# Optimization experiments

Measured on AMD Instinct MI355X. Metric: run time of the kernel, lower is better.

## Reference

```python
import jax, jax.numpy as jnp
import numpy as np
from jax import lax

B, T = 16384, 10
CAR, REG, POI, WEEK, TIME = 500000, 10000, 64, 7, 1440
H, LBL = 256, 512


def setup_inputs() -> dict:
    key = jax.random.key(0)
    ks = jax.random.split(key, 32)
    p = lambda i, shp: jax.random.normal(ks[i], shp, jnp.float32) * 0.05
    d = {}
    d["region_idx"] = jax.random.randint(ks[0], (B, T), 0, REG)
    d["poi_idx"] = jax.random.randint(ks[1], (B, T), 0, POI)
    d["car_idx"] = jax.random.randint(ks[2], (B,), 0, CAR)
    d["week_idx"] = jax.random.randint(ks[3], (B,), 0, WEEK)
    d["time_idx"] = jax.random.randint(ks[4], (B,), 0, TIME)
    d["coords"] = jax.random.normal(ks[5], (B, T, 2), jnp.float32)
    d["region_tbl"] = p(6, (REG, 8))
    d["poi_tbl"] = p(7, (POI, 4))
    d["car_tbl"] = p(8, (CAR, 16))
    d["week_tbl"] = p(9, (WEEK, 3))
    d["time_tbl"] = p(10, (TIME, 8))
    d["W_rp"] = p(11, (12, 32)); d["b_rp"] = p(12, (32,))
    d["W_co"] = p(13, (2, 8));  d["b_co"] = p(14, (8,))
    d["conv_w"] = p(15, (3, 40, 32)); d["conv_b"] = p(16, (32,))
    # 2-layer LSTM (torch gate order i,f,g,o), input 59, hidden 256
    d["Wih0"] = p(17, (4 * H, 59)); d["Whh0"] = p(18, (4 * H, H))
    d["bih0"] = p(19, (4 * H,));    d["bhh0"] = p(20, (4 * H,))
    d["Wih1"] = p(21, (4 * H, H)); d["Whh1"] = p(22, (4 * H, H))
    d["bih1"] = p(23, (4 * H,));   d["bhh1"] = p(24, (4 * H,))
    d["W1"] = p(25, (H, 512));    d["b1"] = p(26, (512,))
    d["W2"] = p(27, (512, 1024)); d["b2"] = p(28, (1024,))
    d["W3"] = p(29, (1024, LBL)); d["b3"] = p(30, (LBL,))
    return d


def _lstm_layer(x, Wih, Whh, bih, bhh):
    Bx, Hh = x.shape[0], Whh.shape[1]
    bias = bih + bhh

    def step(carry, xt):
        h, c = carry
        g = xt @ Wih.T + h @ Whh.T + bias
        i, f, gg, o = jnp.split(g, 4, axis=-1)
        c = jax.nn.sigmoid(f) * c + jax.nn.sigmoid(i) * jnp.tanh(gg)
        h = jax.nn.sigmoid(o) * jnp.tanh(c)
        return (h, c), h

    h0 = jnp.zeros((Bx, Hh), x.dtype)
    _, hs = lax.scan(step, (h0, h0), jnp.swapaxes(x, 0, 1))
    return jnp.swapaxes(hs, 0, 1)


def reference(region_idx, poi_idx, car_idx, week_idx, time_idx, coords,
              region_tbl, poi_tbl, car_tbl, week_tbl, time_tbl,
              W_rp, b_rp, W_co, b_co, conv_w, conv_b,
              Wih0, Whh0, bih0, bhh0, Wih1, Whh1, bih1, bhh1,
              W1, b1, W2, b2, W3, b3):
    # batched embedding gathers (replaces per-item python-loop lookups)
    rp = jnp.concatenate([region_tbl[region_idx], poi_tbl[poi_idx]], -1)   # [B,T,12]
    nv = jnp.concatenate([rp @ W_rp + b_rp, coords @ W_co + b_co], -1)     # [B,T,40]
    conv = jax.nn.elu(
        lax.conv_general_dilated(nv, conv_w, (1,), 'VALID',
                                 dimension_numbers=('NWC', 'WIO', 'NWC')) + conv_b)  # [B,T-2,32]
    emb = jnp.tanh(jnp.concatenate(
        [car_tbl[car_idx], week_tbl[week_idx], time_tbl[time_idx]], -1))   # [B,27]
    x = jnp.concatenate(
        [conv, jnp.broadcast_to(emb[:, None, :], conv.shape[:2] + (27,))], -1)  # [B,T-2,59]
    h = _lstm_layer(x, Wih0, Whh0, bih0, bhh0)
    h = _lstm_layer(h, Wih1, Whh1, bih1, bhh1)
    last = h[:, -1, :]                                                     # [B,256]
    # nn.Sequential of three Linears with NO activations between
    return ((last @ W1 + b1) @ W2 + b2) @ W3 + b3                          # [B,LBL]
```

## Files before the change

### kernel.cpp

```cpp
#include <hip/hip_runtime.h>
#include <hip/hip_bf16.h>
#include <math.h>

#define B_SZ 16384
#define T_CONV 8
#define HID 256
#define SK 16

typedef __bf16 bf16x8 __attribute__((ext_vector_type(8)));
typedef float f32x4 __attribute__((ext_vector_type(4)));

__device__ __forceinline__ float fsigm(float x) { return 1.f / (1.f + __expf(-x)); }
__device__ __forceinline__ float ftanh(float x) {
    float t = __expf(-2.f * fabsf(x));
    float r = (1.f - t) / (1.f + t);
    return x >= 0.f ? r : -r;
}

#define FB_SAMPLES 4
#define CWS 132
__global__ __launch_bounds__(256) void feature_kernel(
    const int* __restrict__ region_idx, const int* __restrict__ poi_idx,
    const int* __restrict__ car_idx, const int* __restrict__ week_idx,
    const int* __restrict__ time_idx, const float* __restrict__ coords,
    const float* __restrict__ region_tbl, const float* __restrict__ poi_tbl,
    const float* __restrict__ car_tbl, const float* __restrict__ week_tbl,
    const float* __restrict__ time_tbl, const float* __restrict__ W_rp,
    const float* __restrict__ b_rp, const float* __restrict__ W_co,
    const float* __restrict__ b_co, const float* __restrict__ conv_w,
    const float* __restrict__ conv_b, __bf16* __restrict__ Xp)
{
    __shared__ __align__(16) float s_cwT[32][CWS];
    __shared__ __align__(16) float s_nv[FB_SAMPLES][10][40];
    __shared__ float s_emb[FB_SAMPLES][27];
    __shared__ float s_rp[FB_SAMPLES][10][12];

    int tid = threadIdx.x;
    for (int i = tid; i < 3840; i += 256) {
        int o = i & 31, rc = i >> 5;
        s_cwT[o][rc] = conv_w[i];
    }

    int s  = tid >> 6;
    int lt = tid & 63;
    int b  = blockIdx.x * FB_SAMPLES + s;

    if (lt < 27) {
        float v;
        if (lt < 16)      v = car_tbl[(size_t)car_idx[b] * 16 + lt];
        else if (lt < 19) v = week_tbl[week_idx[b] * 3 + (lt - 16)];
        else              v = time_tbl[time_idx[b] * 8 + (lt - 19)];
        s_emb[s][lt] = tanhf(v);
    }
    for (int i = lt; i < 120; i += 64) {
        int t = i / 12, k = i % 12;
        float v;
        if (k < 8) v = region_tbl[(size_t)region_idx[b * 10 + t] * 8 + k];
        else       v = poi_tbl[poi_idx[b * 10 + t] * 4 + (k - 8)];
        s_rp[s][t][k] = v;
    }
    __syncthreads();

    for (int i = lt; i < 400; i += 64) {
        int t = i / 40, j = i % 40;
        float acc;
        if (j < 32) {
            acc = b_rp[j];
            #pragma unroll
            for (int k = 0; k < 12; k++) acc += s_rp[s][t][k] * W_rp[k * 32 + j];
        } else {
            int j2 = j - 32;
            acc = b_co[j2] + coords[(size_t)(b * 10 + t) * 2 + 0] * W_co[j2]
                           + coords[(size_t)(b * 10 + t) * 2 + 1] * W_co[8 + j2];
        }
        s_nv[s][t][j] = acc;
    }
    __syncthreads();

    for (int i = lt; i < 256; i += 64) {
        int t = i >> 5, o = i & 31;
        float4 f4 = make_float4(0.f, 0.f, 0.f, 0.f);
        #pragma unroll
        for (int dt = 0; dt < 3; dt++)
            #pragma unroll
            for (int c4 = 0; c4 < 10; c4++) {
                float4 va = *(const float4*)&s_nv[s][t + dt][c4 * 4];
                float4 vw = *(const float4*)&s_cwT[o][dt * 40 + c4 * 4];
                f4.x += va.x * vw.x; f4.y += va.y * vw.y;
                f4.z += va.z * vw.z; f4.w += va.w * vw.w;
            }
        float acc = conv_b[o] + (f4.x + f4.y) + (f4.z + f4.w);
        acc = acc > 0.f ? acc : expm1f(acc);
        Xp[(size_t)(b * 8 + t) * 64 + o] = (__bf16)acc;
    }
    for (int i = lt; i < 216; i += 64) {
        int t = i / 27, j = i % 27;
        Xp[(size_t)(b * 8 + t) * 64 + 32 + j] = (__bf16)s_emb[s][j];
    }
    for (int i = lt; i < 40; i += 64) {
        int t = i / 5, j = i % 5;
        Xp[(size_t)(b * 8 + t) * 64 + 59 + j] = (__bf16)0.f;
    }
}

#define AST 40
__global__ __launch_bounds__(256, 2) void lstm_fused(
    const __bf16* __restrict__ A1, int lda1, int K1,
    const __bf16* __restrict__ A2, int lda2,
    const __bf16* __restrict__ WS,
    const float* __restrict__ bias, float* __restrict__ cst,
    __bf16* __restrict__ hb,
    int KT, int is_t0)
{
    __shared__ __align__(16) unsigned char smem[2 * 128 * AST * 2];
    __bf16* As = (__bf16*)smem;
    float*  GL = (float*)smem;

    int tid = threadIdx.x;
    int bm  = blockIdx.y * 128;
    int bnf = blockIdx.x * 4;
    int bn  = blockIdx.x * 64;
    int l   = tid & 63;
    int g   = tid >> 6;
    int fr  = l & 15;
    int fo  = (l >> 4) * 8;

    f32x4 acc[8][4] = {};

    int s_row  = tid >> 1;
    int s_half = tid & 1;

    auto asrc = [&](int kt) -> const __bf16* {
        int k0 = kt * 32;
        if (k0 < K1) return A1 + (size_t)(bm + s_row) * lda1 + k0 + s_half * 16;
        return A2 + (size_t)(bm + s_row) * lda2 + (k0 - K1) + s_half * 16;
    };
    const __bf16* wbase = WS + ((size_t)g * 16 + bnf) * 512 + (size_t)l * 8;

    {
        const __bf16* s = asrc(0);
        bf16x8 v0 = *(const bf16x8*)s;
        bf16x8 v1 = *(const bf16x8*)(s + 8);
        *(bf16x8*)&As[s_row * AST + s_half * 16]     = v0;
        *(bf16x8*)&As[s_row * AST + s_half * 16 + 8] = v1;
    }
    bf16x8 bcur[4];
    #pragma unroll
    for (int j = 0; j < 4; j++) bcur[j] = *(const bf16x8*)(wbase + j * 512);

    for (int kt = 0; kt < KT; kt++) {
        int cb = kt & 1;
        bf16x8 bnxt[4], an0, an1;
        if (kt + 1 < KT) {
            const __bf16* s = asrc(kt + 1);
            an0 = *(const bf16x8*)s;
            an1 = *(const bf16x8*)(s + 8);
            const __bf16* wb = wbase + (size_t)(kt + 1) * 32768;
            #pragma unroll
            for (int j = 0; j < 4; j++) bnxt[j] = *(const bf16x8*)(wb + j * 512);
        }
        __syncthreads();
        bf16x8 af[8];
        #pragma unroll
        for (int mf = 0; mf < 8; mf++)
            af[mf] = *(bf16x8*)&As[cb * 128 * AST + (mf * 16 + fr) * AST + fo];
        #pragma unroll
        for (int mf = 0; mf < 8; mf++)
            #pragma unroll
            for (int j = 0; j < 4; j++)
                acc[mf][j] = __builtin_amdgcn_mfma_f32_16x16x32_bf16(
                    af[mf], bcur[j], acc[mf][j], 0, 0, 0);
        if (kt + 1 < KT) {
            *(bf16x8*)&As[(cb ^ 1) * 128 * AST + s_row * AST + s_half * 16]     = an0;
            *(bf16x8*)&As[(cb ^ 1) * 128 * AST + s_row * AST + s_half * 16 + 8] = an1;
            #pragma unroll
            for (int j = 0; j < 4; j++) bcur[j] = bnxt[j];
        }
    }

    int rbase = (l >> 4) * 4;
    int prow  = tid >> 4;
    int pcol  = (tid & 15) * 4;
    f32x4 bs[4];
    #pragma unroll
    for (int gg = 0; gg < 4; gg++)
        bs[gg] = *(const f32x4*)&bias[gg * 256 + bn + pcol];

    #pragma unroll
    for (int mf = 0; mf < 8; mf++) {
        __syncthreads();
        #pragma unroll
        for (int j = 0; j < 4; j++)
            #pragma unroll
            for (int e = 0; e < 4; e++)
                GL[(g * 16 + rbase + e) * 68 + j * 16 + fr] = acc[mf][j][e];
        __syncthreads();

        size_t moff = ((size_t)bm + mf * 16 + prow) * 256 + bn + pcol;
        f32x4 gi = *(f32x4*)&GL[(0 * 16 + prow) * 68 + pcol];
        f32x4 gf = *(f32x4*)&GL[(1 * 16 + prow) * 68 + pcol];
        f32x4 gg = *(f32x4*)&GL[(2 * 16 + prow) * 68 + pcol];
        f32x4 go = *(f32x4*)&GL[(3 * 16 + prow) * 68 + pcol];
        f32x4 cold = {0.f, 0.f, 0.f, 0.f};
        if (!is_t0) cold = *(f32x4*)&cst[moff];
        f32x4 cn;
        union { unsigned short u[4]; unsigned long long v; } hx;
        #pragma unroll
        for (int q = 0; q < 4; q++) {
            float i_ = fsigm(gi[q] + bs[0][q]);
            float f_ = fsigm(gf[q] + bs[1][q]);
            float g_ = ftanh(gg[q] + bs[2][q]);
            float o_ = fsigm(go[q] + bs[3][q]);
            float c_ = f_ * cold[q] + i_ * g_;
            cn[q] = c_;
            float h_ = o_ * ftanh(c_);
            __bf16 hv = (__bf16)h_;
            hx.u[q] = *(unsigned short*)&hv;
        }
        *(f32x4*)&cst[moff] = cn;
        *(unsigned long long*)&hb[moff] = hx.v;
    }
}

__global__ __launch_bounds__(256, 2) void head_mfma(
    const __bf16* __restrict__ A,
    const __bf16* __restrict__ WS,
    const float* __restrict__ bias, float* __restrict__ out)
{
    __shared__ __align__(16) __bf16 As[2][128 * AST];

    int tid = threadIdx.x;
    int bm  = blockIdx.y * 128;
    int l   = tid & 63;
    int wv  = tid >> 6;
    int fr  = l & 15;
    int fo  = (l >> 4) * 8;
    int nfb = blockIdx.x * 16 + wv * 4;

    f32x4 acc[8][4] = {};

    int s_row  = tid >> 1;
    int s_half = tid & 1;
    const __bf16* abase = A + (size_t)(bm + s_row) * 256 + s_half * 16;
    const __bf16* wbase = WS + (size_t)nfb * 512 + (size_t)l * 8;

    {
        bf16x8 v0 = *(const bf16x8*)abase;
        bf16x8 v1 = *(const bf16x8*)(abase + 8);
        *(bf16x8*)&As[0][s_row * AST + s_half * 16]     = v0;
        *(bf16x8*)&As[0][s_row * AST + s_half * 16 + 8] = v1;
    }
    bf16x8 bcur[4];
    #pragma unroll
    for (int j = 0; j < 4; j++) bcur[j] = *(const bf16x8*)(wbase + j * 512);

    #pragma unroll
    for (int kt = 0; kt < 8; kt++) {
        int cb = kt & 1;
        bf16x8 bnxt[4], an0, an1;
        if (kt + 1 < 8) {
            const __bf16* s = abase + (kt + 1) * 32;
            an0 = *(const bf16x8*)s;
            an1 = *(const bf16x8*)(s + 8);
            const __bf16* wb = wbase + (size_t)(kt + 1) * 16384;
            #pragma unroll
            for (int j = 0; j < 4; j++) bnxt[j] = *(const bf16x8*)(wb + j * 512);
        }
        __syncthreads();
        bf16x8 af[8];
        #pragma unroll
        for (int mf = 0; mf < 8; mf++)
            af[mf] = *(bf16x8*)&As[cb][(mf * 16 + fr) * AST + fo];
        #pragma unroll
        for (int mf = 0; mf < 8; mf++)
            #pragma unroll
            for (int j = 0; j < 4; j++)
                acc[mf][j] = __builtin_amdgcn_mfma_f32_16x16x32_bf16(
                    af[mf], bcur[j], acc[mf][j], 0, 0, 0);
        if (kt + 1 < 8) {
            *(bf16x8*)&As[cb ^ 1][s_row * AST + s_half * 16]     = an0;
            *(bf16x8*)&As[cb ^ 1][s_row * AST + s_half * 16 + 8] = an1;
            #pragma unroll
            for (int j = 0; j < 4; j++) bcur[j] = bnxt[j];
        }
    }

    int rbase = (l >> 4) * 4;
    #pragma unroll
    for (int mf = 0; mf < 8; mf++) {
        #pragma unroll
        for (int j = 0; j < 4; j++) {
            int n = (nfb + j) * 16 + fr;
            float bv = bias[n];
            #pragma unroll
            for (int e = 0; e < 4; e++) {
                size_t m = (size_t)bm + mf * 16 + rbase + e;
                out[m * 512 + n] = acc[mf][j][e] + bv;
            }
        }
    }
}

__global__ __launch_bounds__(256) void gemm_nn_sk(
    const float* __restrict__ A, int lda, const float* __restrict__ Bm, int ldb,
    float* __restrict__ P, int M, int N, int K)
{
    __shared__ float As[16][68];
    __shared__ float Bs[16][68];
    int tid = threadIdx.x;
    int tx = tid & 15, ty = tid >> 4;
    int bm = blockIdx.y * 64, bn = blockIdx.x * 64;
    int klen = K / SK;
    int kbeg = blockIdx.z * klen;

    float acc[4][4] = {};

    for (int k0 = kbeg; k0 < kbeg + klen; k0 += 16) {
        for (int i = tid; i < 1024; i += 256) {
            int k = i & 15, m = i >> 4;
            As[k][m] = A[(size_t)(bm + m) * lda + k0 + k];
        }
        for (int i = tid; i < 1024; i += 256) {
            int n = i & 63, k = i >> 6;
            Bs[k][n] = Bm[(size_t)(k0 + k) * ldb + bn + n];
        }
        __syncthreads();
        #pragma unroll
        for (int kk = 0; kk < 16; kk++) {
            float4 a = *(const float4*)&As[kk][ty * 4];
            float4 b = *(const float4*)&Bs[kk][tx * 4];
            float av[4] = {a.x, a.y, a.z, a.w};
            float bv[4] = {b.x, b.y, b.z, b.w};
            #pragma unroll
            for (int i = 0; i < 4; i++)
                #pragma unroll
                for (int j = 0; j < 4; j++)
                    acc[i][j] += av[i] * bv[j];
        }
        __syncthreads();
    }

    float* Pd = P + (size_t)blockIdx.z * M * N;
    #pragma unroll
    for (int i = 0; i < 4; i++) {
        int m = bm + ty * 4 + i;
        #pragma unroll
        for (int j = 0; j < 4; j++) {
            int n = bn + tx * 4 + j;
            Pd[(size_t)m * N + n] = acc[i][j];
        }
    }
}

__global__ __launch_bounds__(256) void reduce_sk(
    const float* __restrict__ P, int MN, float* __restrict__ C)
{
    int i = blockIdx.x * 256 + threadIdx.x;
    if (i >= MN) return;
    float a = 0.f;
    #pragma unroll
    for (int s = 0; s < SK; s++) a += P[(size_t)s * MN + i];
    C[i] = a;
}

__global__ __launch_bounds__(256) void vecmat(
    const float* __restrict__ v, const float* __restrict__ M, int ldb, int K,
    const float* __restrict__ bias, float* __restrict__ outv)
{
    __shared__ float red[4][64];
    int l = threadIdx.x & 63;
    int w = threadIdx.x >> 6;
    int n = blockIdx.x * 64 + l;
    int kpw = K >> 2;
    int k0 = w * kpw;

    float p[8] = {};
    for (int k = k0; k < k0 + kpw; k += 8) {
        #pragma unroll
        for (int u = 0; u < 8; u++)
            p[u] += v[k + u] * M[(size_t)(k + u) * ldb + n];
    }
    red[w][l] = ((p[0] + p[1]) + (p[2] + p[3])) + ((p[4] + p[5]) + (p[6] + p[7]));
    __syncthreads();
    if (w == 0)
        outv[n] = red[0][l] + red[1][l] + red[2][l] + red[3][l]
                + (bias ? bias[n] : 0.f);
}

__global__ void add_biases(const float* __restrict__ bih0, const float* __restrict__ bhh0,
                           const float* __restrict__ bih1, const float* __restrict__ bhh1,
                           float* __restrict__ b01)
{
    int i = blockIdx.x * 256 + threadIdx.x;
    if (i < 1024)       b01[i] = bih0[i] + bhh0[i];
    else if (i < 2048)  b01[i] = bih1[i - 1024] + bhh1[i - 1024];
}

__global__ void pack_w01_swz(const float* __restrict__ Wih0, const float* __restrict__ Whh0,
                             const float* __restrict__ Wih1, const float* __restrict__ Whh1,
                             __bf16* __restrict__ WS0, __bf16* __restrict__ WS1)
{
    const int N0 = 10 * 4 * 16 * 64 * 8;
    const int N1 = 16 * 4 * 16 * 64 * 8;
    int idx = blockIdx.x * 256 + threadIdx.x;
    if (idx < N0) {
        int e  = idx & 7;
        int l  = (idx >> 3) & 63;
        int nf = (idx >> 9) & 15;
        int g  = (idx >> 13) & 3;
        int kt = idx >> 15;
        int n_row = g * 256 + nf * 16 + (l & 15);
        int k = kt * 32 + ((l >> 4) * 8) + e;
        float v = (k < 59) ? Wih0[(size_t)n_row * 59 + k]
                : (k < 64) ? 0.f
                           : Whh0[(size_t)n_row * 256 + (k - 64)];
        WS0[idx] = (__bf16)v;
    } else if (idx < N0 + N1) {
        int j = idx - N0;
        int e  = j & 7;
        int l  = (j >> 3) & 63;
        int nf = (j >> 9) & 15;
        int g  = (j >> 13) & 3;
        int kt = j >> 15;
        int n_row = g * 256 + nf * 16 + (l & 15);
        int k = kt * 32 + ((l >> 4) * 8) + e;
        float v = (k < 256) ? Wih1[(size_t)n_row * 256 + k]
                            : Whh1[(size_t)n_row * 256 + (k - 256)];
        WS1[j] = (__bf16)v;
    }
}

__global__ void pack_head_swz(const float* __restrict__ Wc, __bf16* __restrict__ WS)
{
    int idx = blockIdx.x * 256 + threadIdx.x;
    if (idx >= 8 * 32 * 64 * 8) return;
    int e  = idx & 7;
    int l  = (idx >> 3) & 63;
    int nf = (idx >> 9) & 31;
    int kt = idx >> 14;
    int n = nf * 16 + (l & 15);
    int k = kt * 32 + ((l >> 4) * 8) + e;
    WS[idx] = (__bf16)Wc[(size_t)k * 512 + n];
}

extern "C" void kernel_launch(void* const* d_in, const int* in_sizes, int n_in,
                              void* d_out, int out_size, void* d_ws, size_t ws_size,
                              hipStream_t stream)
{
    const int*   region_idx = (const int*)d_in[0];
    const int*   poi_idx    = (const int*)d_in[1];
    const int*   car_idx    = (const int*)d_in[2];
    const int*   week_idx   = (const int*)d_in[3];
    const int*   time_idx   = (const int*)d_in[4];
    const float* coords     = (const float*)d_in[5];
    const float* region_tbl = (const float*)d_in[6];
    const float* poi_tbl    = (const float*)d_in[7];
    const float* car_tbl    = (const float*)d_in[8];
    const float* week_tbl   = (const float*)d_in[9];
    const float* time_tbl   = (const float*)d_in[10];
    const float* W_rp   = (const float*)d_in[11];
    const float* b_rp   = (const float*)d_in[12];
    const float* W_co   = (const float*)d_in[13];
    const float* b_co   = (const float*)d_in[14];
    const float* conv_w = (const float*)d_in[15];
    const float* conv_b = (const float*)d_in[16];
    const float* Wih0 = (const float*)d_in[17];
    const float* Whh0 = (const float*)d_in[18];
    const float* bih0 = (const float*)d_in[19];
    const float* bhh0 = (const float*)d_in[20];
    const float* Wih1 = (const float*)d_in[21];
    const float* Whh1 = (const float*)d_in[22];
    const float* bih1 = (const float*)d_in[23];
    const float* bhh1 = (const float*)d_in[24];
    const float* W1 = (const float*)d_in[25];
    const float* b1 = (const float*)d_in[26];
    const float* W2 = (const float*)d_in[27];
    const float* b2 = (const float*)d_in[28];
    const float* W3 = (const float*)d_in[29];
    const float* b3 = (const float*)d_in[30];
    float* out = (float*)d_out;

    char* ws = (char*)d_ws;
    size_t off = 0;
    auto alloc = [&](size_t bytes) -> char* {
        char* p = ws + off;
        off = (off + bytes + 255) & ~(size_t)255;
        return p;
    };
    __bf16* Xp   = (__bf16*)alloc((size_t)B_SZ * 8 * 64 * 2);
    __bf16* h0b  = (__bf16*)alloc((size_t)B_SZ * HID * 2);
    __bf16* h1b  = (__bf16*)alloc((size_t)B_SZ * HID * 2);
    float*  c0   = (float*)alloc((size_t)B_SZ * HID * 4);
    float*  c1   = (float*)alloc((size_t)B_SZ * HID * 4);
    __bf16* WS0  = (__bf16*)alloc((size_t)10 * 4 * 16 * 64 * 8 * 2);
    __bf16* WS1  = (__bf16*)alloc((size_t)16 * 4 * 16 * 64 * 8 * 2);
    __bf16* WSH  = (__bf16*)alloc((size_t)8 * 32 * 64 * 8 * 2);
    float*  T1    = (float*)alloc(256 * 1024 * 4);
    float*  tb1   = (float*)alloc(1024 * 4);
    float*  Wcomb = (float*)alloc(256 * 512 * 4);
    float*  bcomb = (float*)alloc(512 * 4);
    float*  b01   = (float*)alloc(2048 * 4);
    float*  Psk   = (float*)alloc((size_t)SK * 256 * 1024 * 4);
    (void)ws_size;
    float* bias0 = b01;
    float* bias1 = b01 + 1024;

    pack_w01_swz<<<3328, 256, 0, stream>>>(Wih0, Whh0, Wih1, Whh1, WS0, WS1);
    add_biases<<<8, 256, 0, stream>>>(bih0, bhh0, bih1, bhh1, b01);

    gemm_nn_sk<<<dim3(16, 4, SK), 256, 0, stream>>>(W1, 512, W2, 1024, Psk, 256, 1024, 512);
    reduce_sk<<<(256 * 1024 + 255) / 256, 256, 0, stream>>>(Psk, 256 * 1024, T1);
    vecmat<<<16, 256, 0, stream>>>(b1, W2, 1024, 512, b2, tb1);
    gemm_nn_sk<<<dim3(8, 4, SK), 256, 0, stream>>>(T1, 1024, W3, 512, Psk, 256, 512, 1024);
    reduce_sk<<<(256 * 512 + 255) / 256, 256, 0, stream>>>(Psk, 256 * 512, Wcomb);
    vecmat<<<8, 256, 0, stream>>>(tb1, W3, 512, 1024, b3, bcomb);
    pack_head_swz<<<512, 256, 0, stream>>>(Wcomb, WSH);

    feature_kernel<<<B_SZ / FB_SAMPLES, 256, 0, stream>>>(
        region_idx, poi_idx, car_idx, week_idx, time_idx, coords,
        region_tbl, poi_tbl, car_tbl, week_tbl, time_tbl,
        W_rp, b_rp, W_co, b_co, conv_w, conv_b, Xp);

    dim3 lstm_grid(4, B_SZ / 128);
    for (int t = 0; t < T_CONV; t++) {
        lstm_fused<<<lstm_grid, 256, 0, stream>>>(
            Xp + (size_t)t * 64, 8 * 64, 64,
            h0b, HID,
            WS0, bias0, c0, h0b,
            t == 0 ? 2 : 10, t == 0);

        lstm_fused<<<lstm_grid, 256, 0, stream>>>(
            h0b, HID, 256,
            h1b, HID,
            WS1, bias1, c1, h1b,
            t == 0 ? 8 : 16, t == 0);
    }

    head_mfma<<<dim3(2, 128), 256, 0, stream>>>(h1b, WSH, bcomb, out);
}
```

Baseline: 625.9 us.

## Precompose conv with projections and load LSTM A-fragments directly into registers

```diff
diff --git a/kernel.cpp b/kernel.cpp
--- a/kernel.cpp
+++ b/kernel.cpp
@@ -17,29 +17,57 @@
     return x >= 0.f ? r : -r;
 }
 
+__global__ void collapse_conv(const float* __restrict__ W_rp, const float* __restrict__ b_rp,
+                              const float* __restrict__ W_co, const float* __restrict__ b_co,
+                              const float* __restrict__ conv_w, const float* __restrict__ conv_b,
+                              float* __restrict__ Crp, float* __restrict__ Cco,
+                              float* __restrict__ cb2)
+{
+    int idx = blockIdx.x * 256 + threadIdx.x;
+    if (idx < 1152) {
+        int o = idx & 31, k = (idx >> 5) % 12, dt = idx / 384;
+        float a = 0.f;
+        for (int c = 0; c < 32; c++) a += W_rp[k * 32 + c] * conv_w[(dt * 40 + c) * 32 + o];
+        Crp[idx] = a;
+    } else if (idx < 1344) {
+        int j = idx - 1152;
+        int o = j & 31, k = (j >> 5) & 1, dt = j / 64;
+        float a = 0.f;
+        for (int c = 0; c < 8; c++) a += W_co[k * 8 + c] * conv_w[(dt * 40 + 32 + c) * 32 + o];
+        Cco[j] = a;
+    } else if (idx < 1376) {
+        int o = idx - 1344;
+        float a = conv_b[o];
+        for (int dt = 0; dt < 3; dt++) {
+            for (int c = 0; c < 32; c++) a += b_rp[c] * conv_w[(dt * 40 + c) * 32 + o];
+            for (int c = 0; c < 8; c++)  a += b_co[c] * conv_w[(dt * 40 + 32 + c) * 32 + o];
+        }
+        cb2[o] = a;
+    }
+}
+
 #define FB_SAMPLES 4
-#define CWS 132
 __global__ __launch_bounds__(256) void feature_kernel(
     const int* __restrict__ region_idx, const int* __restrict__ poi_idx,
     const int* __restrict__ car_idx, const int* __restrict__ week_idx,
     const int* __restrict__ time_idx, const float* __restrict__ coords,
     const float* __restrict__ region_tbl, const float* __restrict__ poi_tbl,
     const float* __restrict__ car_tbl, const float* __restrict__ week_tbl,
-    const float* __restrict__ time_tbl, const float* __restrict__ W_rp,
-    const float* __restrict__ b_rp, const float* __restrict__ W_co,
-    const float* __restrict__ b_co, const float* __restrict__ conv_w,
-    const float* __restrict__ conv_b, __bf16* __restrict__ Xp)
-{
-    __shared__ __align__(16) float s_cwT[32][CWS];
-    __shared__ __align__(16) float s_nv[FB_SAMPLES][10][40];
+    const float* __restrict__ time_tbl,
+    const float* __restrict__ Crp, const float* __restrict__ Cco,
+    const float* __restrict__ cb2, __bf16* __restrict__ Xp)
+{
+    __shared__ float s_crp[1152];
+    __shared__ float s_cco[192];
+    __shared__ float s_cb2[32];
+    __shared__ float s_rp[FB_SAMPLES][10][12];
+    __shared__ float s_co[FB_SAMPLES][10][2];
     __shared__ float s_emb[FB_SAMPLES][27];
-    __shared__ float s_rp[FB_SAMPLES][10][12];
 
     int tid = threadIdx.x;
-    for (int i = tid; i < 3840; i += 256) {
-        int o = i & 31, rc = i >> 5;
-        s_cwT[o][rc] = conv_w[i];
-    }
+    for (int i = tid; i < 1152; i += 256) s_crp[i] = Crp[i];
+    if (tid < 192) s_cco[tid] = Cco[tid];
+    else if (tid < 224) s_cb2[tid - 192] = cb2[tid - 192];
 
     int s  = tid >> 6;
     int lt = tid & 63;
@@ -59,37 +87,23 @@
         else       v = poi_tbl[poi_idx[b * 10 + t] * 4 + (k - 8)];
         s_rp[s][t][k] = v;
     }
-    __syncthreads();
-
-    for (int i = lt; i < 400; i += 64) {
-        int t = i / 40, j = i % 40;
-        float acc;
-        if (j < 32) {
-            acc = b_rp[j];
-            #pragma unroll
-            for (int k = 0; k < 12; k++) acc += s_rp[s][t][k] * W_rp[k * 32 + j];
-        } else {
-            int j2 = j - 32;
-            acc = b_co[j2] + coords[(size_t)(b * 10 + t) * 2 + 0] * W_co[j2]
-                           + coords[(size_t)(b * 10 + t) * 2 + 1] * W_co[8 + j2];
-        }
-        s_nv[s][t][j] = acc;
+    for (int i = lt; i < 20; i += 64) {
+        int t = i >> 1, k = i & 1;
+        s_co[s][t][k] = coords[(size_t)(b * 10 + t) * 2 + k];
     }
     __syncthreads();
 
     for (int i = lt; i < 256; i += 64) {
         int t = i >> 5, o = i & 31;
-        float4 f4 = make_float4(0.f, 0.f, 0.f, 0.f);
-        #pragma unroll
-        for (int dt = 0; dt < 3; dt++)
-            #pragma unroll
-            for (int c4 = 0; c4 < 10; c4++) {
-                float4 va = *(const float4*)&s_nv[s][t + dt][c4 * 4];
-                float4 vw = *(const float4*)&s_cwT[o][dt * 40 + c4 * 4];
-                f4.x += va.x * vw.x; f4.y += va.y * vw.y;
-                f4.z += va.z * vw.z; f4.w += va.w * vw.w;
-            }
-        float acc = conv_b[o] + (f4.x + f4.y) + (f4.z + f4.w);
+        float acc = s_cb2[o];
+        #pragma unroll
+        for (int dt = 0; dt < 3; dt++) {
+            #pragma unroll
+            for (int k = 0; k < 12; k++)
+                acc += s_rp[s][t + dt][k] * s_crp[(dt * 12 + k) * 32 + o];
+            acc += s_co[s][t + dt][0] * s_cco[(dt * 2 + 0) * 32 + o]
+                 + s_co[s][t + dt][1] * s_cco[(dt * 2 + 1) * 32 + o];
+        }
         acc = acc > 0.f ? acc : expm1f(acc);
         Xp[(size_t)(b * 8 + t) * 64 + o] = (__bf16)acc;
     }
@@ -103,18 +117,15 @@
     }
 }
 
-#define AST 40
-__global__ __launch_bounds__(256, 2) void lstm_fused(
-    const __bf16* __restrict__ A1, int lda1, int K1,
+template<int KT, int K1>
+__global__ __launch_bounds__(256, 2) void lstm_fused_t(
+    const __bf16* __restrict__ A1, int lda1,
     const __bf16* __restrict__ A2, int lda2,
     const __bf16* __restrict__ WS,
     const float* __restrict__ bias, float* __restrict__ cst,
-    __bf16* __restrict__ hb,
-    int KT, int is_t0)
-{
-    __shared__ __align__(16) unsigned char smem[2 * 128 * AST * 2];
-    __bf16* As = (__bf16*)smem;
-    float*  GL = (float*)smem;
+    __bf16* __restrict__ hb, int is_t0)
+{
+    __shared__ float GL[4 * 16 * 68];
 
     int tid = threadIdx.x;
     int bm  = blockIdx.y * 128;
@@ -127,55 +138,38 @@
 
     f32x4 acc[8][4] = {};
 
-    int s_row  = tid >> 1;
-    int s_half = tid & 1;
-
-    auto asrc = [&](int kt) -> const __bf16* {
+    const __bf16* wbase = WS + ((size_t)g * 16 + bnf) * 512 + (size_t)l * 8;
+
+    auto loadA = [&](int kt, int mf) -> bf16x8 {
         int k0 = kt * 32;
-        if (k0 < K1) return A1 + (size_t)(bm + s_row) * lda1 + k0 + s_half * 16;
-        return A2 + (size_t)(bm + s_row) * lda2 + (k0 - K1) + s_half * 16;
+        const __bf16* p = (k0 < K1)
+            ? A1 + (size_t)(bm + mf * 16 + fr) * lda1 + k0 + fo
+            : A2 + (size_t)(bm + mf * 16 + fr) * lda2 + (k0 - K1) + fo;
+        return *(const bf16x8*)p;
     };
-    const __bf16* wbase = WS + ((size_t)g * 16 + bnf) * 512 + (size_t)l * 8;
-
-    {
-        const __bf16* s = asrc(0);
-        bf16x8 v0 = *(const bf16x8*)s;
-        bf16x8 v1 = *(const bf16x8*)(s + 8);
-        *(bf16x8*)&As[s_row * AST + s_half * 16]     = v0;
-        *(bf16x8*)&As[s_row * AST + s_half * 16 + 8] = v1;
-    }
-    bf16x8 bcur[4];
-    #pragma unroll
-    for (int j = 0; j < 4; j++) bcur[j] = *(const bf16x8*)(wbase + j * 512);
-
+
+    bf16x8 af[2][8], bq[2][4];
+    #pragma unroll
+    for (int mf = 0; mf < 8; mf++) af[0][mf] = loadA(0, mf);
+    #pragma unroll
+    for (int j = 0; j < 4; j++) bq[0][j] = *(const bf16x8*)(wbase + j * 512);
+
+    #pragma unroll
     for (int kt = 0; kt < KT; kt++) {
-        int cb = kt & 1;
-        bf16x8 bnxt[4], an0, an1;
+        const int cur = kt & 1, nx = cur ^ 1;
         if (kt + 1 < KT) {
-            const __bf16* s = asrc(kt + 1);
-            an0 = *(const bf16x8*)s;
-            an1 = *(const bf16x8*)(s + 8);
-            const __bf16* wb = wbase + (size_t)(kt + 1) * 32768;
-            #pragma unroll
-            for (int j = 0; j < 4; j++) bnxt[j] = *(const bf16x8*)(wb + j * 512);
-        }
-        __syncthreads();
-        bf16x8 af[8];
-        #pragma unroll
-        for (int mf = 0; mf < 8; mf++)
-            af[mf] = *(bf16x8*)&As[cb * 128 * AST + (mf * 16 + fr) * AST + fo];
+            #pragma unroll
+            for (int mf = 0; mf < 8; mf++) af[nx][mf] = loadA(kt + 1, mf);
+            #pragma unroll
+            for (int j = 0; j < 4; j++)
+                bq[nx][j] = *(const bf16x8*)(wbase + (size_t)(kt + 1) * 32768 + j * 512);
+        }
         #pragma unroll
         for (int mf = 0; mf < 8; mf++)
             #pragma unroll
             for (int j = 0; j < 4; j++)
                 acc[mf][j] = __builtin_amdgcn_mfma_f32_16x16x32_bf16(
-                    af[mf], bcur[j], acc[mf][j], 0, 0, 0);
-        if (kt + 1 < KT) {
-            *(bf16x8*)&As[(cb ^ 1) * 128 * AST + s_row * AST + s_half * 16]     = an0;
-            *(bf16x8*)&As[(cb ^ 1) * 128 * AST + s_row * AST + s_half * 16 + 8] = an1;
-            #pragma unroll
-            for (int j = 0; j < 4; j++) bcur[j] = bnxt[j];
-        }
+                    af[cur][mf], bq[cur][j], acc[mf][j], 0, 0, 0);
     }
 
     int rbase = (l >> 4) * 4;
@@ -222,6 +216,7 @@
     }
 }
 
+#define AST 40
 __global__ __launch_bounds__(256, 2) void head_mfma(
     const __bf16* __restrict__ A,
     const __bf16* __restrict__ WS,
@@ -500,6 +495,9 @@
     float*  Wcomb = (float*)alloc(256 * 512 * 4);
     float*  bcomb = (float*)alloc(512 * 4);
     float*  b01   = (float*)alloc(2048 * 4);
+    float*  Crp   = (float*)alloc(1152 * 4);
+    float*  Cco   = (float*)alloc(192 * 4);
+    float*  cb2   = (float*)alloc(32 * 4);
     float*  Psk   = (float*)alloc((size_t)SK * 256 * 1024 * 4);
     (void)ws_size;
     float* bias0 = b01;
@@ -507,6 +505,8 @@
 
     pack_w01_swz<<<3328, 256, 0, stream>>>(Wih0, Whh0, Wih1, Whh1, WS0, WS1);
     add_biases<<<8, 256, 0, stream>>>(bih0, bhh0, bih1, bhh1, b01);
+    collapse_conv<<<6, 256, 0, stream>>>(W_rp, b_rp, W_co, b_co, conv_w, conv_b,
+                                         Crp, Cco, cb2);
 
     gemm_nn_sk<<<dim3(16, 4, SK), 256, 0, stream>>>(W1, 512, W2, 1024, Psk, 256, 1024, 512);
     reduce_sk<<<(256 * 1024 + 255) / 256, 256, 0, stream>>>(Psk, 256 * 1024, T1);
@@ -519,21 +519,21 @@
     feature_kernel<<<B_SZ / FB_SAMPLES, 256, 0, stream>>>(
         region_idx, poi_idx, car_idx, week_idx, time_idx, coords,
         region_tbl, poi_tbl, car_tbl, week_tbl, time_tbl,
-        W_rp, b_rp, W_co, b_co, conv_w, conv_b, Xp);
+        Crp, Cco, cb2, Xp);
 
     dim3 lstm_grid(4, B_SZ / 128);
     for (int t = 0; t < T_CONV; t++) {
-        lstm_fused<<<lstm_grid, 256, 0, stream>>>(
-            Xp + (size_t)t * 64, 8 * 64, 64,
-            h0b, HID,
-            WS0, bias0, c0, h0b,
-            t == 0 ? 2 : 10, t == 0);
-
-        lstm_fused<<<lstm_grid, 256, 0, stream>>>(
-            h0b, HID, 256,
-            h1b, HID,
-            WS1, bias1, c1, h1b,
-            t == 0 ? 8 : 16, t == 0);
+        if (t == 0) {
+            lstm_fused_t<2, 64><<<lstm_grid, 256, 0, stream>>>(
+                Xp, 8 * 64, h0b, HID, WS0, bias0, c0, h0b, 1);
+            lstm_fused_t<8, 256><<<lstm_grid, 256, 0, stream>>>(
+                h0b, HID, h1b, HID, WS1, bias1, c1, h1b, 1);
+        } else {
+            lstm_fused_t<10, 64><<<lstm_grid, 256, 0, stream>>>(
+                Xp + (size_t)t * 64, 8 * 64, h0b, HID, WS0, bias0, c0, h0b, 0);
+            lstm_fused_t<16, 256><<<lstm_grid, 256, 0, stream>>>(
+                h0b, HID, h1b, HID, WS1, bias1, c1, h1b, 0);
+        }
     }
 
     head_mfma<<<dim3(2, 128), 256, 0, stream>>>(h1b, WSH, bcomb, out);
```

Measured after the change: 748.2 us. 19.5% more time.
